# Performance work log

Measured on AMD Instinct MI355X. Metric: run time of the kernel, lower is better.

Reference implementation:

```python
import jax, jax.numpy as jnp
import numpy as np
import math

B, T, D, H = 4, 2048, 1024, 16
DH = D // H


def setup_inputs() -> dict:
    key = jax.random.key(0)
    k1, k2, k3 = jax.random.split(key, 3)
    x = jax.random.normal(k1, (B, T, D), dtype=jnp.float32)
    # causal mask: True = masked (positions j > i)
    attn_mask = jnp.triu(jnp.ones((T, T), dtype=bool), k=1)
    key_padding_mask = jnp.zeros((B, T), dtype=bool)  # no padding
    W_qkv = jax.random.normal(k2, (D, 3 * D), dtype=jnp.float32) / math.sqrt(D)
    W_out = jax.random.normal(k3, (D, D), dtype=jnp.float32) / math.sqrt(D)
    return {"x": x, "W_qkv": W_qkv, "W_out": W_out,
            "attn_mask": attn_mask, "key_padding_mask": key_padding_mask}


def reference(x, W_qkv, W_out, attn_mask, key_padding_mask):
    # qkv projection (bias=False)
    qkv = x @ W_qkv                                   # [B,T,3D]
    q, k, v = jnp.split(qkv, 3, axis=-1)              # each [B,T,D]
    # reshape to heads: [B,H,T,DH]
    q = q.reshape(B, T, H, DH).transpose(0, 2, 1, 3)
    k = k.reshape(B, T, H, DH).transpose(0, 2, 1, 3)
    v = v.reshape(B, T, H, DH).transpose(0, 2, 1, 3)
    scale = 1.0 / math.sqrt(DH)
    scores = jnp.einsum('bhqd,bhkd->bhqk', q, k) * scale   # [B,H,T,T]
    neg_inf = jnp.float32(-jnp.inf)
    scores = jnp.where(attn_mask[None, None, :, :], neg_inf, scores)
    scores = jnp.where(key_padding_mask[:, None, None, :], neg_inf, scores)
    attn = jax.nn.softmax(scores, axis=-1)            # dropout p=0.0 -> identity
    out = jnp.einsum('bhqk,bhkd->bhqd', attn, v)      # [B,H,T,DH]
    out = out.transpose(0, 2, 1, 3).reshape(B, T, D)
    return out @ W_out
```

## Files before the change

kernel.cpp:

```cpp
#include <hip/hip_runtime.h>
#include <hip/hip_bf16.h>

#define Bsz 4
#define T 2048
#define D 1024
#define H 16
#define DH 64

typedef unsigned short u16;
typedef __attribute__((ext_vector_type(8))) __bf16 bf16x8;
typedef __attribute__((ext_vector_type(4))) float f32x4;

__device__ inline u16 f2bf(float f) {
  union { float f; unsigned u; } v; v.f = f;
  unsigned r = (v.u + 0x7FFFu + ((v.u >> 16) & 1u)) >> 16;
  return (u16)r;
}
__device__ inline unsigned pack_bf16(float a, float b) {
  union { float f; unsigned u; } A, B; A.f = a; B.f = b;
  unsigned au = A.u + 0x8000u, bu = B.u + 0x8000u;
  return __builtin_amdgcn_perm(bu, au, 0x07060302);
}

__device__ inline void gll16(const u16* g, u16* l) {
  __builtin_amdgcn_global_load_lds((const __attribute__((address_space(1))) void*)g,
                                   (__attribute__((address_space(3))) void*)l, 16, 0, 0);
}

__global__ __launch_bounds__(256) void convert_f32_bf16(const float* __restrict__ in,
                                                        u16* __restrict__ out, int n4) {
  int i = blockIdx.x * 256 + threadIdx.x;
  if (i < n4) {
    float4 v = reinterpret_cast<const float4*>(in)[i];
    ushort4 o;
    o.x = f2bf(v.x); o.y = f2bf(v.y); o.z = f2bf(v.z); o.w = f2bf(v.w);
    reinterpret_cast<ushort4*>(out)[i] = o;
  }
}

__global__ __launch_bounds__(256) void transpose_f32_bf16(const float* __restrict__ in,
                                                          u16* __restrict__ out, int K, int N) {
  __shared__ float tile[32][33];
  int tx = threadIdx.x & 31, ty = threadIdx.x >> 5;
  int n0 = blockIdx.x * 32, k0 = blockIdx.y * 32;
  #pragma unroll
  for (int i = 0; i < 4; ++i)
    tile[ty + i * 8][tx] = in[(size_t)(k0 + ty + i * 8) * N + n0 + tx];
  __syncthreads();
  #pragma unroll
  for (int i = 0; i < 4; ++i)
    out[(size_t)(n0 + ty + i * 8) * K + k0 + tx] = f2bf(tile[tx][ty + i * 8]);
}

template <int MODE>
__global__ __launch_bounds__(256) void gemm128(const u16* __restrict__ A, const u16* __restrict__ BT,
                                               float* __restrict__ C,
                                               u16* __restrict__ Qh, u16* __restrict__ Kh,
                                               u16* __restrict__ VTh, int M, int N, int K) {
  __shared__ u16 As[128][32];
  __shared__ u16 Bs[128][32];
  int tid = threadIdx.x;
  int m0 = blockIdx.y * 128, n0 = blockIdx.x * 128;
  int w = tid >> 6, lane = tid & 63;
  int llo = lane & 15, lhi = lane >> 4;
  int wm = (w >> 1) * 64, wn = (w & 1) * 64;

  f32x4 acc[4][4];
  #pragma unroll
  for (int i = 0; i < 4; ++i)
    #pragma unroll
    for (int j = 0; j < 4; ++j) acc[i][j] = (f32x4){0.f, 0.f, 0.f, 0.f};

  const u16* gA = A + (size_t)(m0 + w * 32 + (lane >> 2)) * K + (lane & 3) * 8;
  const u16* gB = BT + (size_t)(n0 + w * 32 + (lane >> 2)) * K + (lane & 3) * 8;

  for (int k0 = 0; k0 < K; k0 += 32) {
    gll16(gA + k0, &As[w * 32][0]);
    gll16(gA + (size_t)16 * K + k0, &As[w * 32 + 16][0]);
    gll16(gB + k0, &Bs[w * 32][0]);
    gll16(gB + (size_t)16 * K + k0, &Bs[w * 32 + 16][0]);
    __syncthreads();
    bf16x8 af[4], bfr[4];
    #pragma unroll
    for (int i = 0; i < 4; ++i)
      af[i] = *reinterpret_cast<const bf16x8*>(&As[wm + i * 16 + llo][lhi * 8]);
    #pragma unroll
    for (int j = 0; j < 4; ++j)
      bfr[j] = *reinterpret_cast<const bf16x8*>(&Bs[wn + j * 16 + llo][lhi * 8]);
    #pragma unroll
    for (int i = 0; i < 4; ++i)
      #pragma unroll
      for (int j = 0; j < 4; ++j)
        acc[i][j] = __builtin_amdgcn_mfma_f32_16x16x32_bf16(af[i], bfr[j], acc[i][j], 0, 0, 0);
    __syncthreads();
  }

  if (MODE == 0) {
    #pragma unroll
    for (int i = 0; i < 4; ++i)
      #pragma unroll
      for (int j = 0; j < 4; ++j) {
        int nl = n0 + wn + j * 16 + llo;
        #pragma unroll
        for (int r = 0; r < 4; ++r) {
          int ml = m0 + wm + i * 16 + lhi * 4 + r;
          C[(size_t)ml * N + nl] = acc[i][j][r];
        }
      }
  } else {
    int seg = n0 >> 10;
    #pragma unroll
    for (int i = 0; i < 4; ++i) {
      int mbase = m0 + wm + i * 16 + lhi * 4;
      int t0 = mbase & (T - 1);
      int b_ = mbase >> 11;
      #pragma unroll
      for (int j = 0; j < 4; ++j) {
        int nl = n0 + wn + j * 16 + llo;
        int h = (nl >> 6) & 15, d = nl & 63;
        int bh = b_ * H + h;
        if (seg == 0) {
          #pragma unroll
          for (int r = 0; r < 4; ++r)
            Qh[((size_t)bh * T + t0 + r) * DH + d] = f2bf(acc[i][j][r] * 0.125f);
        } else if (seg == 1) {
          #pragma unroll
          for (int r = 0; r < 4; ++r)
            Kh[((size_t)bh * T + t0 + r) * DH + d] = f2bf(acc[i][j][r]);
        } else {
          uint2 p;
          p.x = pack_bf16(acc[i][j][0], acc[i][j][1]);
          p.y = pack_bf16(acc[i][j][2], acc[i][j][3]);
          *reinterpret_cast<uint2*>(&VTh[((size_t)bh * DH + d) * T + t0]) = p;
        }
      }
    }
  }
}

__global__ __launch_bounds__(512, 4) void attn_fwd(const u16* __restrict__ Qh, const u16* __restrict__ Kh,
                                                   const u16* __restrict__ VTh, u16* __restrict__ AO) {
  __shared__ u16 QP[8][16][72];
  __shared__ u16 Ks[64][72];
  __shared__ u16 Vs[64][72];
  int tid = threadIdx.x;
  int pair = blockIdx.x, bh = blockIdx.y;
  int w = tid >> 6, lane = tid & 63;
  int llo = lane & 15, lhi = lane >> 4;

  int qrow_s = tid >> 2, qc = tid & 3;
  int krow_s = tid >> 3, kc = tid & 7;
  const u16* kbase = Kh + ((size_t)bh * T + krow_s) * DH + kc * 8;
  const u16* vbase = VTh + ((size_t)bh * DH + krow_s) * T + kc * 8;

  #pragma unroll 1
  for (int half = 0; half < 2; ++half) {
    int qt = half ? (15 - pair) : pair;
    __syncthreads();
    {
      const uint4* g = reinterpret_cast<const uint4*>(
          Qh + ((size_t)bh * T + qt * 128 + qrow_s) * DH + qc * 16);
      uint4 a = g[0], b = g[1];
      uint4* dst = reinterpret_cast<uint4*>(&QP[qrow_s >> 4][qrow_s & 15][qc * 16]);
      dst[0] = a; dst[1] = b;
    }
    __syncthreads();

    bf16x8 aq[2];
    #pragma unroll
    for (int ks = 0; ks < 2; ++ks)
      aq[ks] = *reinterpret_cast<const bf16x8*>(&QP[w][llo][ks * 32 + lhi * 8]);

    f32x4 o[4];
    #pragma unroll
    for (int i = 0; i < 4; ++i) o[i] = (f32x4){0.f, 0.f, 0.f, 0.f};
    float l_run = 0.f;

    int nj = 2 * qt + 2;
    #pragma unroll 1
    for (int j = 0; j < nj; ++j) {
      __syncthreads();
      {
        uint4 a = *reinterpret_cast<const uint4*>(kbase + (size_t)j * 64 * DH);
        uint4 b = *reinterpret_cast<const uint4*>(vbase + j * 64);
        *reinterpret_cast<uint4*>(&Ks[krow_s][kc * 8]) = a;
        *reinterpret_cast<uint4*>(&Vs[krow_s][kc * 8]) = b;
      }
      __syncthreads();

      f32x4 sc[4];
      #pragma unroll
      for (int kt = 0; kt < 4; ++kt) {
        bf16x8 bk0 = *reinterpret_cast<const bf16x8*>(&Ks[kt * 16 + llo][lhi * 8]);
        bf16x8 bk1 = *reinterpret_cast<const bf16x8*>(&Ks[kt * 16 + llo][32 + lhi * 8]);
        f32x4 z = (f32x4){0.f, 0.f, 0.f, 0.f};
        f32x4 t0 = __builtin_amdgcn_mfma_f32_16x16x32_bf16(bk0, aq[0], z, 0, 0, 0);
        sc[kt] = __builtin_amdgcn_mfma_f32_16x16x32_bf16(bk1, aq[1], t0, 0, 0, 0);
      }

      if (j >= 2 * qt) {
        int qrow_g = qt * 128 + w * 16 + llo;
        #pragma unroll
        for (int kt = 0; kt < 4; ++kt)
          #pragma unroll
          for (int r = 0; r < 4; ++r) {
            int key_g = j * 64 + kt * 16 + lhi * 4 + r;
            if (key_g > qrow_g) sc[kt][r] = -__builtin_inff();
          }
      }

      float s_sum = 0.f;
      #pragma unroll
      for (int kt = 0; kt < 4; ++kt)
        #pragma unroll
        for (int r = 0; r < 4; ++r) {
          float p = __expf(sc[kt][r]);
          sc[kt][r] = p;
          s_sum += p;
        }
      s_sum += __shfl_xor(s_sum, 16);
      s_sum += __shfl_xor(s_sum, 32);
      l_run += s_sum;

      #pragma unroll
      for (int kt = 0; kt < 4; ++kt) {
        uint2 p;
        p.x = pack_bf16(sc[kt][0], sc[kt][1]);
        p.y = pack_bf16(sc[kt][2], sc[kt][3]);
        *reinterpret_cast<uint2*>(&QP[w][llo][kt * 16 + lhi * 4]) = p;
      }

      #pragma unroll
      for (int kk2 = 0; kk2 < 2; ++kk2) {
        bf16x8 pa = *reinterpret_cast<const bf16x8*>(&QP[w][llo][kk2 * 32 + lhi * 8]);
        #pragma unroll
        for (int nt = 0; nt < 4; ++nt) {
          bf16x8 bv = *reinterpret_cast<const bf16x8*>(&Vs[nt * 16 + llo][kk2 * 32 + lhi * 8]);
          o[nt] = __builtin_amdgcn_mfma_f32_16x16x32_bf16(pa, bv, o[nt], 0, 0, 0);
        }
      }
    }

    int b = bh >> 4, h = bh & 15;
    #pragma unroll
    for (int r = 0; r < 4; ++r) {
      float inv = 1.f / __shfl(l_run, lhi * 4 + r);
      int t = qt * 128 + w * 16 + lhi * 4 + r;
      #pragma unroll
      for (int nt = 0; nt < 4; ++nt)
        AO[((size_t)(b * T + t)) * D + h * 64 + nt * 16 + llo] = f2bf(o[nt][r] * inv);
    }
  }
}

extern "C" void kernel_launch(void* const* d_in, const int* in_sizes, int n_in,
                              void* d_out, int out_size, void* d_ws, size_t ws_size,
                              hipStream_t stream) {
  (void)in_sizes; (void)n_in; (void)out_size;
  const float* x = (const float*)d_in[0];
  const float* Wqkv = (const float*)d_in[1];
  const float* Wout = (const float*)d_in[2];
  float* out = (float*)d_out;

  char* ws = (char*)d_ws;
  size_t off = 0;
  u16* xb = (u16*)(ws + off);    off += (size_t)Bsz * T * D * 2;
  u16* WqkvT = (u16*)(ws + off); off += (size_t)3 * D * D * 2;
  u16* WoutT = (u16*)(ws + off); off += (size_t)D * D * 2;
  u16* Qh = (u16*)(ws + off);    off += (size_t)Bsz * H * T * DH * 2;
  u16* Kh = (u16*)(ws + off);    off += (size_t)Bsz * H * T * DH * 2;
  u16* VTh = (u16*)(ws + off);   off += (size_t)Bsz * H * DH * T * 2;
  u16* AO = xb;
  if (ws_size < off) return;

  int n4 = Bsz * T * D / 4;
  convert_f32_bf16<<<(n4 + 255) / 256, 256, 0, stream>>>(x, xb, n4);
  transpose_f32_bf16<<<dim3(3 * D / 32, D / 32), 256, 0, stream>>>(Wqkv, WqkvT, D, 3 * D);
  transpose_f32_bf16<<<dim3(D / 32, D / 32), 256, 0, stream>>>(Wout, WoutT, D, D);
  gemm128<1><<<dim3(3 * D / 128, Bsz * T / 128), 256, 0, stream>>>(xb, WqkvT, nullptr, Qh, Kh, VTh,
                                                                   Bsz * T, 3 * D, D);
  attn_fwd<<<dim3(T / 256, Bsz * H), 512, 0, stream>>>(Qh, Kh, VTh, AO);
  gemm128<0><<<dim3(D / 128, Bsz * T / 128), 256, 0, stream>>>(AO, WoutT, out, nullptr, nullptr, nullptr,
                                                               Bsz * T, D, D);
}
```

Before: 283.3 us.

## Process contiguous 256-row query tiles per block sharing K/V loads, prefetch next tile

The attention kernel now has each block own one contiguous 256-row query tile, split into two 128-row subtiles held in registers. Before, a block handled two paired 128-row tiles one after the other. Each K/V tile staged in shared memory is now used by both subtiles, which roughly halves K/V global traffic and barrier count. The next K/V tile is also prefetched into registers while the current one is consumed. In exchange, per-block work now varies with the causal position, so there is load imbalance; blocks are launched heaviest-first to soften it. Register pressure is higher from the doubled accumulators.

```diff
diff --git a/kernel.cpp b/kernel.cpp
--- a/kernel.cpp
+++ b/kernel.cpp
@@ -144,62 +144,69 @@
   __shared__ u16 Ks[64][72];
   __shared__ u16 Vs[64][72];
   int tid = threadIdx.x;
-  int pair = blockIdx.x, bh = blockIdx.y;
+  int qtile = 7 - blockIdx.x, bh = blockIdx.y;
   int w = tid >> 6, lane = tid & 63;
   int llo = lane & 15, lhi = lane >> 4;
+  int q0 = qtile * 256;
 
   int qrow_s = tid >> 2, qc = tid & 3;
   int krow_s = tid >> 3, kc = tid & 7;
   const u16* kbase = Kh + ((size_t)bh * T + krow_s) * DH + kc * 8;
   const u16* vbase = VTh + ((size_t)bh * DH + krow_s) * T + kc * 8;
 
+  bf16x8 aq[2][2];
+  #pragma unroll
+  for (int s = 0; s < 2; ++s) {
+    const uint4* g = reinterpret_cast<const uint4*>(
+        Qh + ((size_t)bh * T + q0 + s * 128 + qrow_s) * DH + qc * 16);
+    uint4 a = g[0], b = g[1];
+    uint4* dst = reinterpret_cast<uint4*>(&QP[w][qrow_s & 15][qc * 16]);
+    dst[0] = a; dst[1] = b;
+    #pragma unroll
+    for (int ks = 0; ks < 2; ++ks)
+      aq[s][ks] = *reinterpret_cast<const bf16x8*>(&QP[w][llo][ks * 32 + lhi * 8]);
+  }
+
+  f32x4 o[2][4];
+  float l_run[2];
+  #pragma unroll
+  for (int s = 0; s < 2; ++s) {
+    l_run[s] = 0.f;
+    #pragma unroll
+    for (int i = 0; i < 4; ++i) o[s][i] = (f32x4){0.f, 0.f, 0.f, 0.f};
+  }
+
+  int nj = 4 * qtile + 4;
+  uint4 ka = *reinterpret_cast<const uint4*>(kbase);
+  uint4 va = *reinterpret_cast<const uint4*>(vbase);
+
   #pragma unroll 1
-  for (int half = 0; half < 2; ++half) {
-    int qt = half ? (15 - pair) : pair;
-    __syncthreads();
-    {
-      const uint4* g = reinterpret_cast<const uint4*>(
-          Qh + ((size_t)bh * T + qt * 128 + qrow_s) * DH + qc * 16);
-      uint4 a = g[0], b = g[1];
-      uint4* dst = reinterpret_cast<uint4*>(&QP[qrow_s >> 4][qrow_s & 15][qc * 16]);
-      dst[0] = a; dst[1] = b;
-    }
-    __syncthreads();
-
-    bf16x8 aq[2];
-    #pragma unroll
-    for (int ks = 0; ks < 2; ++ks)
-      aq[ks] = *reinterpret_cast<const bf16x8*>(&QP[w][llo][ks * 32 + lhi * 8]);
-
-    f32x4 o[4];
-    #pragma unroll
-    for (int i = 0; i < 4; ++i) o[i] = (f32x4){0.f, 0.f, 0.f, 0.f};
-    float l_run = 0.f;
-
-    int nj = 2 * qt + 2;
+  for (int j = 0; j < nj; ++j) {
+    __syncthreads();
+    *reinterpret_cast<uint4*>(&Ks[krow_s][kc * 8]) = ka;
+    *reinterpret_cast<uint4*>(&Vs[krow_s][kc * 8]) = va;
+    if (j + 1 < nj) {
+      ka = *reinterpret_cast<const uint4*>(kbase + (size_t)(j + 1) * 64 * DH);
+      va = *reinterpret_cast<const uint4*>(vbase + (j + 1) * 64);
+    }
+    __syncthreads();
+
+    int smax = (j < 4 * qtile + 2) ? 2 : 1;
     #pragma unroll 1
-    for (int j = 0; j < nj; ++j) {
-      __syncthreads();
-      {
-        uint4 a = *reinterpret_cast<const uint4*>(kbase + (size_t)j * 64 * DH);
-        uint4 b = *reinterpret_cast<const uint4*>(vbase + j * 64);
-        *reinterpret_cast<uint4*>(&Ks[krow_s][kc * 8]) = a;
-        *reinterpret_cast<uint4*>(&Vs[krow_s][kc * 8]) = b;
-      }
-      __syncthreads();
-
+    for (int si = 0; si < smax; ++si) {
+      int s = (smax == 1) ? 1 : si;
       f32x4 sc[4];
       #pragma unroll
       for (int kt = 0; kt < 4; ++kt) {
         bf16x8 bk0 = *reinterpret_cast<const bf16x8*>(&Ks[kt * 16 + llo][lhi * 8]);
         bf16x8 bk1 = *reinterpret_cast<const bf16x8*>(&Ks[kt * 16 + llo][32 + lhi * 8]);
         f32x4 z = (f32x4){0.f, 0.f, 0.f, 0.f};
-        f32x4 t0 = __builtin_amdgcn_mfma_f32_16x16x32_bf16(bk0, aq[0], z, 0, 0, 0);
-        sc[kt] = __builtin_amdgcn_mfma_f32_16x16x32_bf16(bk1, aq[1], t0, 0, 0, 0);
-      }
-
-      if (j >= 2 * qt) {
-        int qrow_g = qt * 128 + w * 16 + llo;
+        f32x4 t0 = __builtin_amdgcn_mfma_f32_16x16x32_bf16(bk0, aq[s][0], z, 0, 0, 0);
+        sc[kt] = __builtin_amdgcn_mfma_f32_16x16x32_bf16(bk1, aq[s][1], t0, 0, 0, 0);
+      }
+
+      if (j >= 4 * qtile + 2 * s) {
+        int qrow_g = q0 + s * 128 + w * 16 + llo;
         #pragma unroll
         for (int kt = 0; kt < 4; ++kt)
           #pragma unroll
@@ -220,7 +227,7 @@
         }
       s_sum += __shfl_xor(s_sum, 16);
       s_sum += __shfl_xor(s_sum, 32);
-      l_run += s_sum;
+      l_run[s] += s_sum;
 
       #pragma unroll
       for (int kt = 0; kt < 4; ++kt) {
@@ -236,21 +243,23 @@
         #pragma unroll
         for (int nt = 0; nt < 4; ++nt) {
           bf16x8 bv = *reinterpret_cast<const bf16x8*>(&Vs[nt * 16 + llo][kk2 * 32 + lhi * 8]);
-          o[nt] = __builtin_amdgcn_mfma_f32_16x16x32_bf16(pa, bv, o[nt], 0, 0, 0);
-        }
-      }
-    }
-
-    int b = bh >> 4, h = bh & 15;
+          o[s][nt] = __builtin_amdgcn_mfma_f32_16x16x32_bf16(pa, bv, o[s][nt], 0, 0, 0);
+        }
+      }
+    }
+  }
+
+  int b = bh >> 4, h = bh & 15;
+  #pragma unroll
+  for (int s = 0; s < 2; ++s)
     #pragma unroll
     for (int r = 0; r < 4; ++r) {
-      float inv = 1.f / __shfl(l_run, lhi * 4 + r);
-      int t = qt * 128 + w * 16 + lhi * 4 + r;
+      float inv = 1.f / __shfl(l_run[s], lhi * 4 + r);
+      int t = q0 + s * 128 + w * 16 + lhi * 4 + r;
       #pragma unroll
       for (int nt = 0; nt < 4; ++nt)
-        AO[((size_t)(b * T + t)) * D + h * 64 + nt * 16 + llo] = f2bf(o[nt][r] * inv);
-    }
-  }
+        AO[((size_t)(b * T + t)) * D + h * 64 + nt * 16 + llo] = f2bf(o[s][nt][r] * inv);
+    }
 }
 
 extern "C" void kernel_launch(void* const* d_in, const int* in_sizes, int n_in,
@@ -279,7 +288,7 @@
   transpose_f32_bf16<<<dim3(D / 32, D / 32), 256, 0, stream>>>(Wout, WoutT, D, D);
   gemm128<1><<<dim3(3 * D / 128, Bsz * T / 128), 256, 0, stream>>>(xb, WqkvT, nullptr, Qh, Kh, VTh,
                                                                    Bsz * T, 3 * D, D);
-  attn_fwd<<<dim3(T / 256, Bsz * H), 512, 0, stream>>>(Qh, Kh, VTh, AO);
+  attn_fwd<<<dim3(8, Bsz * H), 512, 0, stream>>>(Qh, Kh, VTh, AO);
   gemm128<0><<<dim3(D / 128, Bsz * T / 128), 256, 0, stream>>>(AO, WoutT, out, nullptr, nullptr, nullptr,
                                                                Bsz * T, D, D);
 }
```

Measured after the change: 507.6 us. 1.79x slower.

## Enlarge attention tile to 256 queries per 1024-thread block with register-prefetched K/V

Applied to the files above, without the earlier changes.

The attention kernel now uses 16 waves of 1024 threads, each block covering a 256-row query tile, so every K/V tile loaded into LDS serves twice as many query rows. The next K/V tile is prefetched into registers while the current one is consumed. Waves whose rows lie fully above the causal diagonal skip the MFMA and softmax work. The trade-off is a grid of only 256 blocks, fewer than before, which may hurt occupancy and load balance, and each barrier now syncs 16 waves.

```diff
diff --git a/kernel.cpp b/kernel.cpp
--- a/kernel.cpp
+++ b/kernel.cpp
@@ -138,114 +138,121 @@
   }
 }
 
-__global__ __launch_bounds__(512, 4) void attn_fwd(const u16* __restrict__ Qh, const u16* __restrict__ Kh,
-                                                   const u16* __restrict__ VTh, u16* __restrict__ AO) {
-  __shared__ u16 QP[8][16][72];
+__global__ __launch_bounds__(1024, 4) void attn_fwd(const u16* __restrict__ Qh, const u16* __restrict__ Kh,
+                                                    const u16* __restrict__ VTh, u16* __restrict__ AO) {
+  __shared__ u16 QP[16][16][72];
   __shared__ u16 Ks[64][72];
   __shared__ u16 Vs[64][72];
   int tid = threadIdx.x;
-  int pair = blockIdx.x, bh = blockIdx.y;
+  int qp = blockIdx.x, bh = blockIdx.y;
   int w = tid >> 6, lane = tid & 63;
   int llo = lane & 15, lhi = lane >> 4;
 
   int qrow_s = tid >> 2, qc = tid & 3;
-  int krow_s = tid >> 3, kc = tid & 7;
-  const u16* kbase = Kh + ((size_t)bh * T + krow_s) * DH + kc * 8;
-  const u16* vbase = VTh + ((size_t)bh * DH + krow_s) * T + kc * 8;
+  int krow_s = tid >> 4, kc = tid & 15;
+  const u16* kbase = Kh + ((size_t)bh * T + krow_s) * DH + kc * 4;
+  const u16* vbase = VTh + ((size_t)bh * DH + krow_s) * T + kc * 4;
+  int b = bh >> 4, h = bh & 15;
 
   #pragma unroll 1
   for (int half = 0; half < 2; ++half) {
-    int qt = half ? (15 - pair) : pair;
-    __syncthreads();
+    int qt = half ? (7 - qp) : qp;
+    int q0 = qt * 256;
+
+    bf16x8 aq[2];
     {
       const uint4* g = reinterpret_cast<const uint4*>(
-          Qh + ((size_t)bh * T + qt * 128 + qrow_s) * DH + qc * 16);
-      uint4 a = g[0], b = g[1];
-      uint4* dst = reinterpret_cast<uint4*>(&QP[qrow_s >> 4][qrow_s & 15][qc * 16]);
-      dst[0] = a; dst[1] = b;
-    }
-    __syncthreads();
-
-    bf16x8 aq[2];
-    #pragma unroll
-    for (int ks = 0; ks < 2; ++ks)
-      aq[ks] = *reinterpret_cast<const bf16x8*>(&QP[w][llo][ks * 32 + lhi * 8]);
+          Qh + ((size_t)bh * T + q0 + qrow_s) * DH + qc * 16);
+      uint4 a = g[0], bb = g[1];
+      uint4* dst = reinterpret_cast<uint4*>(&QP[w][qrow_s & 15][qc * 16]);
+      dst[0] = a; dst[1] = bb;
+      #pragma unroll
+      for (int ks = 0; ks < 2; ++ks)
+        aq[ks] = *reinterpret_cast<const bf16x8*>(&QP[w][llo][ks * 32 + lhi * 8]);
+    }
 
     f32x4 o[4];
     #pragma unroll
     for (int i = 0; i < 4; ++i) o[i] = (f32x4){0.f, 0.f, 0.f, 0.f};
     float l_run = 0.f;
 
-    int nj = 2 * qt + 2;
+    int nj = 4 * qt + 4;
+    uint2 ka = *reinterpret_cast<const uint2*>(kbase);
+    uint2 va = *reinterpret_cast<const uint2*>(vbase);
+
     #pragma unroll 1
     for (int j = 0; j < nj; ++j) {
       __syncthreads();
-      {
-        uint4 a = *reinterpret_cast<const uint4*>(kbase + (size_t)j * 64 * DH);
-        uint4 b = *reinterpret_cast<const uint4*>(vbase + j * 64);
-        *reinterpret_cast<uint4*>(&Ks[krow_s][kc * 8]) = a;
-        *reinterpret_cast<uint4*>(&Vs[krow_s][kc * 8]) = b;
+      *reinterpret_cast<uint2*>(&Ks[krow_s][kc * 4]) = ka;
+      *reinterpret_cast<uint2*>(&Vs[krow_s][kc * 4]) = va;
+      if (j + 1 < nj) {
+        ka = *reinterpret_cast<const uint2*>(kbase + (size_t)(j + 1) * 64 * DH);
+        va = *reinterpret_cast<const uint2*>(vbase + (j + 1) * 64);
+      } else if (half == 0) {
+        ka = *reinterpret_cast<const uint2*>(kbase);
+        va = *reinterpret_cast<const uint2*>(vbase);
       }
       __syncthreads();
 
-      f32x4 sc[4];
-      #pragma unroll
-      for (int kt = 0; kt < 4; ++kt) {
-        bf16x8 bk0 = *reinterpret_cast<const bf16x8*>(&Ks[kt * 16 + llo][lhi * 8]);
-        bf16x8 bk1 = *reinterpret_cast<const bf16x8*>(&Ks[kt * 16 + llo][32 + lhi * 8]);
-        f32x4 z = (f32x4){0.f, 0.f, 0.f, 0.f};
-        f32x4 t0 = __builtin_amdgcn_mfma_f32_16x16x32_bf16(bk0, aq[0], z, 0, 0, 0);
-        sc[kt] = __builtin_amdgcn_mfma_f32_16x16x32_bf16(bk1, aq[1], t0, 0, 0, 0);
-      }
-
-      if (j >= 2 * qt) {
-        int qrow_g = qt * 128 + w * 16 + llo;
+      if (q0 + w * 16 + 15 >= j * 64) {
+        f32x4 sc[4];
+        #pragma unroll
+        for (int kt = 0; kt < 4; ++kt) {
+          bf16x8 bk0 = *reinterpret_cast<const bf16x8*>(&Ks[kt * 16 + llo][lhi * 8]);
+          bf16x8 bk1 = *reinterpret_cast<const bf16x8*>(&Ks[kt * 16 + llo][32 + lhi * 8]);
+          f32x4 z = (f32x4){0.f, 0.f, 0.f, 0.f};
+          f32x4 t0 = __builtin_amdgcn_mfma_f32_16x16x32_bf16(bk0, aq[0], z, 0, 0, 0);
+          sc[kt] = __builtin_amdgcn_mfma_f32_16x16x32_bf16(bk1, aq[1], t0, 0, 0, 0);
+        }
+
+        if (j >= 4 * qt) {
+          int qrow_g = q0 + w * 16 + llo;
+          #pragma unroll
+          for (int kt = 0; kt < 4; ++kt)
+            #pragma unroll
+            for (int r = 0; r < 4; ++r) {
+              int key_g = j * 64 + kt * 16 + lhi * 4 + r;
+              if (key_g > qrow_g) sc[kt][r] = -__builtin_inff();
+            }
+        }
+
+        float s_sum = 0.f;
         #pragma unroll
         for (int kt = 0; kt < 4; ++kt)
           #pragma unroll
           for (int r = 0; r < 4; ++r) {
-            int key_g = j * 64 + kt * 16 + lhi * 4 + r;
-            if (key_g > qrow_g) sc[kt][r] = -__builtin_inff();
+            float p = __expf(sc[kt][r]);
+            sc[kt][r] = p;
+            s_sum += p;
           }
-      }
-
-      float s_sum = 0.f;
-      #pragma unroll
-      for (int kt = 0; kt < 4; ++kt)
-        #pragma unroll
-        for (int r = 0; r < 4; ++r) {
-          float p = __expf(sc[kt][r]);
-          sc[kt][r] = p;
-          s_sum += p;
-        }
-      s_sum += __shfl_xor(s_sum, 16);
-      s_sum += __shfl_xor(s_sum, 32);
-      l_run += s_sum;
-
-      #pragma unroll
-      for (int kt = 0; kt < 4; ++kt) {
-        uint2 p;
-        p.x = pack_bf16(sc[kt][0], sc[kt][1]);
-        p.y = pack_bf16(sc[kt][2], sc[kt][3]);
-        *reinterpret_cast<uint2*>(&QP[w][llo][kt * 16 + lhi * 4]) = p;
-      }
-
-      #pragma unroll
-      for (int kk2 = 0; kk2 < 2; ++kk2) {
-        bf16x8 pa = *reinterpret_cast<const bf16x8*>(&QP[w][llo][kk2 * 32 + lhi * 8]);
-        #pragma unroll
-        for (int nt = 0; nt < 4; ++nt) {
-          bf16x8 bv = *reinterpret_cast<const bf16x8*>(&Vs[nt * 16 + llo][kk2 * 32 + lhi * 8]);
-          o[nt] = __builtin_amdgcn_mfma_f32_16x16x32_bf16(pa, bv, o[nt], 0, 0, 0);
-        }
-      }
-    }
-
-    int b = bh >> 4, h = bh & 15;
+        s_sum += __shfl_xor(s_sum, 16);
+        s_sum += __shfl_xor(s_sum, 32);
+        l_run += s_sum;
+
+        #pragma unroll
+        for (int kt = 0; kt < 4; ++kt) {
+          uint2 p;
+          p.x = pack_bf16(sc[kt][0], sc[kt][1]);
+          p.y = pack_bf16(sc[kt][2], sc[kt][3]);
+          *reinterpret_cast<uint2*>(&QP[w][llo][kt * 16 + lhi * 4]) = p;
+        }
+
+        #pragma unroll
+        for (int kk2 = 0; kk2 < 2; ++kk2) {
+          bf16x8 pa = *reinterpret_cast<const bf16x8*>(&QP[w][llo][kk2 * 32 + lhi * 8]);
+          #pragma unroll
+          for (int nt = 0; nt < 4; ++nt) {
+            bf16x8 bv = *reinterpret_cast<const bf16x8*>(&Vs[nt * 16 + llo][kk2 * 32 + lhi * 8]);
+            o[nt] = __builtin_amdgcn_mfma_f32_16x16x32_bf16(pa, bv, o[nt], 0, 0, 0);
+          }
+        }
+      }
+    }
+
     #pragma unroll
     for (int r = 0; r < 4; ++r) {
       float inv = 1.f / __shfl(l_run, lhi * 4 + r);
-      int t = qt * 128 + w * 16 + lhi * 4 + r;
+      int t = q0 + w * 16 + lhi * 4 + r;
       #pragma unroll
       for (int nt = 0; nt < 4; ++nt)
         AO[((size_t)(b * T + t)) * D + h * 64 + nt * 16 + llo] = f2bf(o[nt][r] * inv);
@@ -279,7 +286,7 @@
   transpose_f32_bf16<<<dim3(D / 32, D / 32), 256, 0, stream>>>(Wout, WoutT, D, D);
   gemm128<1><<<dim3(3 * D / 128, Bsz * T / 128), 256, 0, stream>>>(xb, WqkvT, nullptr, Qh, Kh, VTh,
                                                                    Bsz * T, 3 * D, D);
-  attn_fwd<<<dim3(T / 256, Bsz * H), 512, 0, stream>>>(Qh, Kh, VTh, AO);
+  attn_fwd<<<dim3(4, Bsz * H), 1024, 0, stream>>>(Qh, Kh, VTh, AO);
   gemm128<0><<<dim3(D / 128, Bsz * T / 128), 256, 0, stream>>>(AO, WoutT, out, nullptr, nullptr, nullptr,
                                                                Bsz * T, D, D);
 }
```

Measured after the change: 278.0 us. No clear change (-1.9%).
